# Performance work log

Measured on AMD Instinct MI355X. Metric: run time of the kernel, lower is better.

Reference implementation:

```python
import jax, jax.numpy as jnp
import numpy as np

# static config
B, L, D = 2, 4096, 1024
H, G, WIN = 16, 2, 256
HD = D // H            # 64
KV = G * HD            # 128 (k/v proj width)
E, HID, TOPK = 8, 1024, 2
ENT_W, MAX_USE, EPS = 0.05, 0.4, 1e-8


def setup_inputs() -> dict:
    key = jax.random.key(0)
    ks = jax.random.split(key, 16)
    s = 0.02
    return {
        "x": jax.random.normal(ks[0], (B, L, D), jnp.float32),
        "Wq": jax.random.normal(ks[1], (D, D), jnp.float32) * s,
        "bq": jnp.zeros((D,), jnp.float32),
        "Wk": jax.random.normal(ks[2], (D, KV), jnp.float32) * s,
        "bk": jnp.zeros((KV,), jnp.float32),
        "Wv": jax.random.normal(ks[3], (D, KV), jnp.float32) * s,
        "bv": jnp.zeros((KV,), jnp.float32),
        "Wo": jax.random.normal(ks[4], (D, D), jnp.float32) * s,
        "bo": jnp.zeros((D,), jnp.float32),
        "ln1_g": jnp.ones((D,), jnp.float32),
        "ln1_b": jnp.zeros((D,), jnp.float32),
        "ln2_g": jnp.ones((D,), jnp.float32),
        "ln2_b": jnp.zeros((D,), jnp.float32),
        "Wg": jax.random.normal(ks[5], (D, E), jnp.float32) * 0.01,
        "bg": jnp.zeros((E,), jnp.float32),
        "We": jax.random.normal(ks[6], (E, D, HID), jnp.float32) * s,
        "be": jnp.zeros((E, HID), jnp.float32),
    }


def _layernorm(x, g, b):
    mu = jnp.mean(x, axis=-1, keepdims=True)
    var = jnp.var(x, axis=-1, keepdims=True)
    return (x - mu) * jax.lax.rsqrt(var + 1e-5) * g + b


def _local_attn(x, Wq, bq, Wk, bk, Wv, bv, Wo, bo):
    # overlapping sliding-window bidirectional GQA attention (dropout off / eval)
    Bx, Lx, _ = x.shape
    pad = (-Lx) % WIN
    xp = jnp.pad(x, ((0, 0), (0, pad), (0, 0)))
    Lp = Lx + pad
    q = (xp @ Wq + bq).reshape(Bx, Lp, H, HD).transpose(0, 2, 1, 3)   # [B,H,Lp,hd]
    k = (xp @ Wk + bk).reshape(Bx, Lp, G, HD).transpose(0, 2, 1, 3)   # [B,G,Lp,hd]
    v = (xp @ Wv + bv).reshape(Bx, Lp, G, HD).transpose(0, 2, 1, 3)
    stride = WIN // 2
    nw = (Lp - WIN) // stride + 1
    win_idx = (np.arange(nw)[:, None] * stride + np.arange(WIN)[None, :])
    qw = q[:, :, win_idx]
    kw = k[:, :, win_idx]
    vw = v[:, :, win_idx]
    rep = H // G
    # torch .repeat tiles kv groups: head h uses group h % G, i.e. h = r*G + g
    qw = qw.reshape(Bx, rep, G, nw, WIN, HD)
    scores = jnp.einsum('brgnqd,bgnkd->brgnqk', qw, kw) / np.sqrt(HD)
    attn = jax.nn.softmax(scores, axis=-1)
    o = jnp.einsum('brgnqk,bgnkd->brgnqd', attn, vw)
    o = o.reshape(Bx, H, nw, WIN, HD).transpose(0, 2, 3, 1, 4).reshape(Bx, nw * WIN, D)
    o = o[:, :Lx]                             # truncate concatenated windows to L
    return o @ Wo + bo


def _moe(x, Wg, bg, We, be):
    Bx, Lx, _ = x.shape
    xf = x.reshape(-1, D)                     # [N,D]
    N = xf.shape[0]
    probs = jax.nn.softmax(xf @ Wg + bg, axis=-1)          # [N,E]
    entropy = -jnp.sum(probs * jnp.log(probs + EPS), axis=-1).mean()
    ent_loss = ENT_W * entropy
    topk_p, topk_i = jax.lax.top_k(probs, TOPK)            # [N,K]
    # dense grouped-GEMM reference for top-k dispatch/combine
    all_out = jnp.einsum('nd,edh->neh', xf, We) + be       # [N,E,HID]
    wts = jnp.zeros((N, E), xf.dtype).at[jnp.arange(N)[:, None], topk_i].add(topk_p)
    out = jnp.einsum('ne,neh->nh', wts, all_out)           # [N,HID]
    counts = jnp.zeros((E,), xf.dtype).at[topk_i.reshape(-1)].add(1.0)
    usage = counts / (N + EPS)
    penalty = jnp.sum(jax.nn.relu(usage - MAX_USE))
    return out.reshape(Bx, Lx, HID), ent_loss + penalty


def reference(x, Wq, bq, Wk, bk, Wv, bv, Wo, bo, ln1_g, ln1_b, ln2_g, ln2_b, Wg, bg, We, be):
    h = x + _local_attn(_layernorm(x, ln1_g, ln1_b), Wq, bq, Wk, bk, Wv, bv, Wo, bo)
    moe_out, aux = _moe(_layernorm(h, ln2_g, ln2_b), Wg, bg, We, be)
    out = h + moe_out
    return out, aux
```

## Files before the change

### kernel.cpp

```cpp
#include <hip/hip_runtime.h>
#include <hip/hip_bf16.h>
#include <stdint.h>

typedef __attribute__((ext_vector_type(8))) short bf16x8;
typedef __attribute__((ext_vector_type(8))) _Float16 f16x8;
typedef __attribute__((ext_vector_type(4))) _Float16 f16x4;
typedef __attribute__((ext_vector_type(4))) float f32x4;

__device__ __forceinline__ short f2bf(float f) {
  __hip_bfloat16 h = __float2bfloat16(f);
  union { __hip_bfloat16 h; short s; } u; u.h = h; return u.s;
}

__device__ __forceinline__ unsigned pk2(float a, float b) {
  union { _Float16 h; unsigned short s; } ua, ub;
  ua.h = (_Float16)a; ub.h = (_Float16)b;
  return (unsigned)ua.s | ((unsigned)ub.s << 16);
}

__device__ __forceinline__ void gld16(const void* g, void* l) {
  __builtin_amdgcn_global_load_lds((const __attribute__((address_space(1))) void*)g,
                                   (__attribute__((address_space(3))) void*)l, 16, 0, 0);
}

__device__ __forceinline__ float wave_sum64(float v) {
  #pragma unroll
  for (int off = 1; off < 64; off <<= 1) v += __shfl_xor(v, off);
  return v;
}
__device__ __forceinline__ double wave_sum64d(double v) {
  #pragma unroll
  for (int off = 1; off < 64; off <<= 1) v += __shfl_xor(v, off);
  return v;
}

__global__ __launch_bounds__(256) void ln_split(const float* __restrict__ x,
    const float* __restrict__ g, const float* __restrict__ b,
    _Float16* __restrict__ xh, _Float16* __restrict__ xl) {
  int t = blockIdx.x, tid = threadIdx.x;
  const float4 v = ((const float4*)(x + (size_t)t * 1024))[tid];
  float s = v.x + v.y + v.z + v.w;
  float s2 = v.x*v.x + v.y*v.y + v.z*v.z + v.w*v.w;
  s = wave_sum64(s); s2 = wave_sum64(s2);
  __shared__ float pa[4], pb[4];
  int wid = tid >> 6, lane = tid & 63;
  if (lane == 0) { pa[wid] = s; pb[wid] = s2; }
  __syncthreads();
  float S = pa[0]+pa[1]+pa[2]+pa[3], S2 = pb[0]+pb[1]+pb[2]+pb[3];
  float mu = S * (1.f/1024.f);
  float var = S2 * (1.f/1024.f) - mu*mu;
  float rs = rsqrtf(var + 1e-5f);
  const float4 gv = ((const float4*)g)[tid];
  const float4 bv = ((const float4*)b)[tid];
  float4 o;
  o.x = (v.x-mu)*rs*gv.x + bv.x; o.y = (v.y-mu)*rs*gv.y + bv.y;
  o.z = (v.z-mu)*rs*gv.z + bv.z; o.w = (v.w-mu)*rs*gv.w + bv.w;
  f16x4 hv, lv;
  hv.x = (_Float16)o.x; lv.x = (_Float16)((o.x - (float)hv.x)*2048.f);
  hv.y = (_Float16)o.y; lv.y = (_Float16)((o.y - (float)hv.y)*2048.f);
  hv.z = (_Float16)o.z; lv.z = (_Float16)((o.z - (float)hv.z)*2048.f);
  hv.w = (_Float16)o.w; lv.w = (_Float16)((o.w - (float)hv.w)*2048.f);
  *(f16x4*)&xh[(size_t)t*1024 + tid*4] = hv;
  *(f16x4*)&xl[(size_t)t*1024 + tid*4] = lv;
}

__global__ __launch_bounds__(256) void ln_bf16(const float* __restrict__ x,
    const float* __restrict__ g, const float* __restrict__ b, short* __restrict__ out,
    float2* __restrict__ murs) {
  int t = blockIdx.x, tid = threadIdx.x;
  const float4 v = ((const float4*)(x + (size_t)t * 1024))[tid];
  float s = v.x + v.y + v.z + v.w;
  float s2 = v.x*v.x + v.y*v.y + v.z*v.z + v.w*v.w;
  s = wave_sum64(s); s2 = wave_sum64(s2);
  __shared__ float pa[4], pb[4];
  int wid = tid >> 6, lane = tid & 63;
  if (lane == 0) { pa[wid] = s; pb[wid] = s2; }
  __syncthreads();
  float S = pa[0]+pa[1]+pa[2]+pa[3], S2 = pb[0]+pb[1]+pb[2]+pb[3];
  float mu = S * (1.f/1024.f);
  float var = S2 * (1.f/1024.f) - mu*mu;
  float rs = rsqrtf(var + 1e-5f);
  if (tid == 0) murs[t] = make_float2(mu, rs);
  const float4 gv = ((const float4*)g)[tid];
  const float4 bv = ((const float4*)b)[tid];
  short4 o;
  o.x = f2bf((v.x-mu)*rs*gv.x + bv.x); o.y = f2bf((v.y-mu)*rs*gv.y + bv.y);
  o.z = f2bf((v.z-mu)*rs*gv.z + bv.z); o.w = f2bf((v.w-mu)*rs*gv.w + bv.w);
  ((short4*)(out + (size_t)t * 1024))[tid] = o;
}

__global__ void t_w_f16(const float* __restrict__ src, int srcN,
                        _Float16* __restrict__ dh, _Float16* __restrict__ dl, int dstRow0) {
  __shared__ float tile[32][33];
  int kt = blockIdx.x, nt = blockIdx.y;
  int tx = threadIdx.x, ty = threadIdx.y;
  #pragma unroll
  for (int i = 0; i < 4; i++)
    tile[ty + 8*i][tx] = src[(size_t)(kt*32 + ty + 8*i)*srcN + nt*32 + tx];
  __syncthreads();
  #pragma unroll
  for (int i = 0; i < 4; i++) {
    float v = tile[tx][ty + 8*i];
    _Float16 h = (_Float16)v;
    _Float16 l = (_Float16)((v - (float)h) * 2048.0f);
    size_t o = (size_t)(dstRow0 + nt*32 + ty + 8*i)*1024 + kt*32 + tx;
    dh[o] = h; dl[o] = l;
  }
}

template<int MODE>
__global__ __launch_bounds__(256, 3) void gemm_dma(
    const _Float16* __restrict__ Agh, const _Float16* __restrict__ Agl,
    const _Float16* __restrict__ BTh, const _Float16* __restrict__ BTl,
    const float* __restrict__ b0, const float* __restrict__ b1, const float* __restrict__ b2,
    const float* __restrict__ resid,
    float* __restrict__ out0, float* __restrict__ out1, float* __restrict__ out2) {
  int m0 = blockIdx.x * 64;
  int y = blockIdx.y;
  int n0 = y * 128;
  float* dst; const float* biasp; int dcol0, ld;
  if (MODE == 0) {
    if (y < 8)      { dst = out0; biasp = b0 + y*128; dcol0 = y*128; ld = 1024; }
    else if (y == 8){ dst = out1; biasp = b1; dcol0 = 0; ld = 128; }
    else            { dst = out2; biasp = b2; dcol0 = 0; ld = 128; }
  } else            { dst = out0; biasp = b0 + y*128; dcol0 = y*128; ld = 1024; }

  __shared__ _Float16 AhS[2][2048];
  __shared__ _Float16 AlS[2][2048];
  __shared__ _Float16 BhS[2][4096];
  __shared__ _Float16 BlS[2][4096];
  int tid = threadIdx.x;
  int lane = tid & 63, w = tid >> 6;
  int wm = (w & 1) * 32, wn = (w >> 1) * 64;
  int l15 = lane & 15, quad = lane >> 4;

  int Pa = tid;
  int cA = (Pa & 3) ^ ((Pa >> 4) & 3);
  size_t gA = (size_t)(m0 + (Pa >> 2)) * 1024 + cA * 8;
  int Pb0 = tid, Pb1 = tid + 256;
  int cB0 = (Pb0 & 3) ^ ((Pb0 >> 4) & 3);
  int cB1 = (Pb1 & 3) ^ ((Pb1 >> 4) & 3);
  size_t gB0 = (size_t)(n0 + (Pb0 >> 2)) * 1024 + cB0 * 8;
  size_t gB1 = (size_t)(n0 + (Pb1 >> 2)) * 1024 + cB1 * 8;

  f32x4 accM[2][4] = {};
  f32x4 accC[2][4] = {};

  gld16(Agh + gA, &AhS[0][Pa*8]);
  gld16(Agl + gA, &AlS[0][Pa*8]);
  gld16(BTh + gB0, &BhS[0][Pb0*8]);
  gld16(BTh + gB1, &BhS[0][Pb1*8]);
  gld16(BTl + gB0, &BlS[0][Pb0*8]);
  gld16(BTl + gB1, &BlS[0][Pb1*8]);
  __syncthreads();

  int cur = 0;
  for (int it = 0; it < 32; ++it) {
    if (it < 31) {
      int kb = (it + 1) * 32;
      int nb = cur ^ 1;
      gld16(Agh + gA + kb, &AhS[nb][Pa*8]);
      gld16(Agl + gA + kb, &AlS[nb][Pa*8]);
      gld16(BTh + gB0 + kb, &BhS[nb][Pb0*8]);
      gld16(BTh + gB1 + kb, &BhS[nb][Pb1*8]);
      gld16(BTl + gB0 + kb, &BlS[nb][Pb0*8]);
      gld16(BTl + gB1 + kb, &BlS[nb][Pb1*8]);
    }
    f16x8 bh[4], bl[4];
    #pragma unroll
    for (int nt = 0; nt < 4; nt++) {
      int row = wn + nt*16 + l15;
      int pc = quad ^ ((row >> 2) & 3);
      bh[nt] = *(const f16x8*)&BhS[cur][row*32 + pc*8];
      bl[nt] = *(const f16x8*)&BlS[cur][row*32 + pc*8];
    }
    #pragma unroll
    for (int mt = 0; mt < 2; mt++) {
      int row = wm + mt*16 + l15;
      int pc = quad ^ ((row >> 2) & 3);
      f16x8 ah = *(const f16x8*)&AhS[cur][row*32 + pc*8];
      f16x8 al = *(const f16x8*)&AlS[cur][row*32 + pc*8];
      #pragma unroll
      for (int nt = 0; nt < 4; nt++) {
        accM[mt][nt] = __builtin_amdgcn_mfma_f32_16x16x32_f16(ah, bh[nt], accM[mt][nt], 0, 0, 0);
        accC[mt][nt] = __builtin_amdgcn_mfma_f32_16x16x32_f16(ah, bl[nt], accC[mt][nt], 0, 0, 0);
        accC[mt][nt] = __builtin_amdgcn_mfma_f32_16x16x32_f16(al, bh[nt], accC[mt][nt], 0, 0, 0);
      }
    }
    __syncthreads();
    cur ^= 1;
  }

  const float inv2048 = 1.0f / 2048.0f;
  #pragma unroll
  for (int mt = 0; mt < 2; mt++)
    #pragma unroll
    for (int r = 0; r < 4; r++) {
      int row = m0 + wm + mt*16 + quad*4 + r;
      #pragma unroll
      for (int nt = 0; nt < 4; nt++) {
        int c = wn + nt*16 + l15;
        float v = accM[mt][nt][r] + accC[mt][nt][r]*inv2048 + biasp[c];
        if (MODE == 1) v += resid[(size_t)row*1024 + dcol0 + c];
        dst[(size_t)row*ld + dcol0 + c] = v;
      }
    }
}

__global__ __launch_bounds__(256, 2) void attn_mfma(
    const float* __restrict__ Qs, const float* __restrict__ Kf, const float* __restrict__ Vf,
    _Float16* __restrict__ Oh, _Float16* __restrict__ Ol) {
  int qb = blockIdx.x, n = blockIdx.y;
  int b = blockIdx.z >> 4, h = blockIdx.z & 15;
  int g = h & 1;
  int tid = threadIdx.x;
  int lane = tid & 63, w = tid >> 6;
  int l15 = lane & 15, quad = lane >> 4;

  __shared__ __align__(16) char smem[70912];
  _Float16* Vt = (_Float16*)smem;
  _Float16* Qh = (_Float16*)(smem + 33792);
  _Float16* Ql = (_Float16*)(smem + 43008);
  _Float16* Kh = (_Float16*)(smem + 52224);
  _Float16* Kl = (_Float16*)(smem + 61440);
  _Float16* Pm = (_Float16*)(smem + 33792);
  float*   linv = (float*)(smem + 70656);

  int qtok0 = b*4096 + n*128 + qb*64;
  int key0  = b*4096 + n*128;

  #pragma unroll
  for (int i = 0; i < 4; i++) {
    int idx = tid + 256*i;
    int row = idx >> 4, c4 = idx & 15;
    float4 v = *(const float4*)&Qs[(size_t)(qtok0+row)*1024 + h*64 + c4*4];
    f16x4 hv, lv;
    hv.x = (_Float16)v.x; lv.x = (_Float16)(v.x - (float)hv.x);
    hv.y = (_Float16)v.y; lv.y = (_Float16)(v.y - (float)hv.y);
    hv.z = (_Float16)v.z; lv.z = (_Float16)(v.z - (float)hv.z);
    hv.w = (_Float16)v.w; lv.w = (_Float16)(v.w - (float)hv.w);
    *(f16x4*)&Qh[row*72 + c4*4] = hv;
    *(f16x4*)&Ql[row*72 + c4*4] = lv;
  }
  {
    int kk = tid >> 4, dd = tid & 15;
    #pragma unroll
    for (int i = 0; i < 8; i++) {
      int p = i*16 + kk;
      float4 v0 = *(const float4*)&Vf[(size_t)(key0 + 2*p    )*128 + g*64 + dd*4];
      float4 v1 = *(const float4*)&Vf[(size_t)(key0 + 2*p + 1)*128 + g*64 + dd*4];
      *(unsigned*)&Vt[(dd*4+0)*264 + 2*p] = pk2(v0.x, v1.x);
      *(unsigned*)&Vt[(dd*4+1)*264 + 2*p] = pk2(v0.y, v1.y);
      *(unsigned*)&Vt[(dd*4+2)*264 + 2*p] = pk2(v0.z, v1.z);
      *(unsigned*)&Vt[(dd*4+3)*264 + 2*p] = pk2(v0.w, v1.w);
    }
  }
  __syncthreads();

  f16x8 qh[2], ql[2];
  {
    int qrow = (w*16 + l15)*72;
    qh[0] = *(const f16x8*)&Qh[qrow + quad*8];
    qh[1] = *(const f16x8*)&Qh[qrow + 32 + quad*8];
    ql[0] = *(const f16x8*)&Ql[qrow + quad*8];
    ql[1] = *(const f16x8*)&Ql[qrow + 32 + quad*8];
  }

  f32x4 S[16];
  #pragma unroll
  for (int t = 0; t < 16; t++) S[t] = (f32x4){0.f,0.f,0.f,0.f};

  for (int c = 0; c < 4; c++) {
    if (c) __syncthreads();
    #pragma unroll
    for (int i = 0; i < 4; i++) {
      int idx = tid + 256*i;
      int row = idx >> 4, c4 = idx & 15;
      float4 v = *(const float4*)&Kf[(size_t)(key0 + c*64 + row)*128 + g*64 + c4*4];
      f16x4 hv, lv;
      hv.x = (_Float16)v.x; lv.x = (_Float16)(v.x - (float)hv.x);
      hv.y = (_Float16)v.y; lv.y = (_Float16)(v.y - (float)hv.y);
      hv.z = (_Float16)v.z; lv.z = (_Float16)(v.z - (float)hv.z);
      hv.w = (_Float16)v.w; lv.w = (_Float16)(v.w - (float)hv.w);
      *(f16x4*)&Kh[row*72 + c4*4] = hv;
      *(f16x4*)&Kl[row*72 + c4*4] = lv;
    }
    __syncthreads();
    #pragma unroll
    for (int t = 0; t < 4; t++) {
      int krow = (t*16 + l15)*72;
      f16x8 kh0 = *(const f16x8*)&Kh[krow + quad*8];
      f16x8 kh1 = *(const f16x8*)&Kh[krow + 32 + quad*8];
      f16x8 kl0 = *(const f16x8*)&Kl[krow + quad*8];
      f16x8 kl1 = *(const f16x8*)&Kl[krow + 32 + quad*8];
      int ti = c*4 + t;
      S[ti] = __builtin_amdgcn_mfma_f32_16x16x32_f16(qh[0], kh0, S[ti], 0, 0, 0);
      S[ti] = __builtin_amdgcn_mfma_f32_16x16x32_f16(ql[0], kh0, S[ti], 0, 0, 0);
      S[ti] = __builtin_amdgcn_mfma_f32_16x16x32_f16(qh[0], kl0, S[ti], 0, 0, 0);
      S[ti] = __builtin_amdgcn_mfma_f32_16x16x32_f16(qh[1], kh1, S[ti], 0, 0, 0);
      S[ti] = __builtin_amdgcn_mfma_f32_16x16x32_f16(ql[1], kh1, S[ti], 0, 0, 0);
      S[ti] = __builtin_amdgcn_mfma_f32_16x16x32_f16(qh[1], kl1, S[ti], 0, 0, 0);
    }
  }

  float lrow[4];
  #pragma unroll
  for (int r = 0; r < 4; r++) {
    float mx = S[0][r];
    #pragma unroll
    for (int t = 1; t < 16; t++) mx = fmaxf(mx, S[t][r]);
    mx = fmaxf(mx, __shfl_xor(mx, 1)); mx = fmaxf(mx, __shfl_xor(mx, 2));
    mx = fmaxf(mx, __shfl_xor(mx, 4)); mx = fmaxf(mx, __shfl_xor(mx, 8));
    float sum = 0.f;
    #pragma unroll
    for (int t = 0; t < 16; t++) {
      float e = __expf((S[t][r] - mx) * 0.125f);
      S[t][r] = e; sum += e;
    }
    sum += __shfl_xor(sum, 1); sum += __shfl_xor(sum, 2);
    sum += __shfl_xor(sum, 4); sum += __shfl_xor(sum, 8);
    lrow[r] = sum;
  }
  if (l15 == 0) {
    #pragma unroll
    for (int r = 0; r < 4; r++) linv[w*16 + quad*4 + r] = 1.f / lrow[r];
  }
  __syncthreads();

  #pragma unroll
  for (int r = 0; r < 4; r++) {
    int q = w*16 + quad*4 + r;
    bool mine = (l15 & 1) ? (r >= 2) : (r < 2);
    #pragma unroll
    for (int t = 0; t < 16; t++) {
      float own = S[t][r];
      float oth = __shfl_xor(own, 1);
      if (mine) {
        float e0 = (l15 & 1) ? oth : own;
        float e1 = (l15 & 1) ? own : oth;
        *(unsigned*)&Pm[q*264 + t*16 + (l15 & ~1)] = pk2(e0, e1);
      }
    }
  }
  __syncthreads();

  f32x4 O[4];
  #pragma unroll
  for (int t = 0; t < 4; t++) O[t] = (f32x4){0.f,0.f,0.f,0.f};
  {
    int prow = (w*16 + l15)*264;
    #pragma unroll
    for (int ks = 0; ks < 8; ks++) {
      f16x8 pa = *(const f16x8*)&Pm[prow + ks*32 + quad*8];
      #pragma unroll
      for (int t = 0; t < 4; t++) {
        f16x8 vb = *(const f16x8*)&Vt[(t*16 + l15)*264 + ks*32 + quad*8];
        O[t] = __builtin_amdgcn_mfma_f32_16x16x32_f16(pa, vb, O[t], 0, 0, 0);
      }
    }
  }

  #pragma unroll
  for (int r = 0; r < 4; r++) {
    int qlocal = w*16 + quad*4 + r;
    float inv = linv[qlocal];
    int orow = b*4096 + n*256 + qb*64 + qlocal;
    #pragma unroll
    for (int t = 0; t < 4; t++) {
      float o = O[t][r] * inv;
      _Float16 oh = (_Float16)o;
      _Float16 ol = (_Float16)((o - (float)oh) * 2048.f);
      size_t oo = (size_t)orow*1024 + h*64 + t*16 + l15;
      Oh[oo] = oh; Ol[oo] = ol;
    }
  }
}

__global__ __launch_bounds__(256) void gating_logits(
    const float* __restrict__ h, const float2* __restrict__ murs,
    const float* __restrict__ g2, const float* __restrict__ b2,
    const float* __restrict__ Wg, const float* __restrict__ bg,
    int* __restrict__ e1e2, float2* __restrict__ p12, float* __restrict__ entArr) {
  int tid = threadIdx.x, lane = tid & 63, wid = tid >> 6;
  int tok = blockIdx.x*4 + wid;
  const float* row = h + (size_t)tok * 1024;
  float2 mr = murs[tok];
  double mu = (double)mr.x, rs = (double)mr.y;
  double acc[8] = {};
  #pragma unroll
  for (int q = 0; q < 4; q++) {
    float4 xv = ((const float4*)row)[lane*4 + q];
    float4 gv = ((const float4*)g2)[lane*4 + q];
    float4 bv = ((const float4*)b2)[lane*4 + q];
    float xs[4] = {xv.x, xv.y, xv.z, xv.w};
    float gs[4] = {gv.x, gv.y, gv.z, gv.w};
    float bs[4] = {bv.x, bv.y, bv.z, bv.w};
    #pragma unroll
    for (int j = 0; j < 4; j++) {
      int i = lane*16 + q*4 + j;
      double xn = ((double)xs[j] - mu) * rs * (double)gs[j] + (double)bs[j];
      const float4 w0 = *(const float4*)&Wg[(size_t)i*8];
      const float4 w1 = *(const float4*)&Wg[(size_t)i*8 + 4];
      acc[0] += xn*(double)w0.x; acc[1] += xn*(double)w0.y;
      acc[2] += xn*(double)w0.z; acc[3] += xn*(double)w0.w;
      acc[4] += xn*(double)w1.x; acc[5] += xn*(double)w1.y;
      acc[6] += xn*(double)w1.z; acc[7] += xn*(double)w1.w;
    }
  }
  #pragma unroll
  for (int e = 0; e < 8; e++) acc[e] = wave_sum64d(acc[e]) + (double)bg[e];
  int e1 = 0;
  #pragma unroll
  for (int e = 1; e < 8; e++) if (acc[e] > acc[e1]) e1 = e;
  int e2 = (e1 == 0) ? 1 : 0;
  #pragma unroll
  for (int e = 0; e < 8; e++) if (e != e1 && acc[e] > acc[e2]) e2 = e;
  float lf[8];
  #pragma unroll
  for (int e = 0; e < 8; e++) lf[e] = (float)acc[e];
  float mx = lf[0];
  #pragma unroll
  for (int e = 1; e < 8; e++) mx = fmaxf(mx, lf[e]);
  float ex[8], Z = 0.f;
  #pragma unroll
  for (int e = 0; e < 8; e++) { ex[e] = __expf(lf[e] - mx); Z += ex[e]; }
  float invZ = 1.f / Z, ent = 0.f;
  float p[8];
  #pragma unroll
  for (int e = 0; e < 8; e++) { p[e] = ex[e]*invZ; ent -= p[e]*__logf(p[e] + 1e-8f); }
  if (lane == 0) {
    e1e2[tok] = e1 | (e2 << 8);
    p12[tok]  = make_float2(p[e1], p[e2]);
    entArr[tok] = ent;
  }
}

__global__ __launch_bounds__(128) void scatter_kernel(
    const int* __restrict__ e1e2, const float2* __restrict__ p12,
    int* __restrict__ cnt, int* __restrict__ bucket, float* __restrict__ bucketP,
    int* __restrict__ bucketS) {
  __shared__ int lcnt[8], base[8];
  int tid = threadIdx.x;
  if (tid < 8) lcnt[tid] = 0;
  __syncthreads();
  int tok = blockIdx.x*128 + tid;
  int ee = e1e2[tok];
  int e1 = ee & 255, e2 = ee >> 8;
  float2 p = p12[tok];
  int o1 = atomicAdd(&lcnt[e1], 1);
  int o2 = atomicAdd(&lcnt[e2], 1);
  __syncthreads();
  if (tid < 8) base[tid] = atomicAdd(&cnt[tid], lcnt[tid]);
  __syncthreads();
  int i1 = base[e1] + o1;
  bucket[e1*8192 + i1] = tok; bucketP[e1*8192 + i1] = p.x; bucketS[e1*8192 + i1] = 0;
  int i2 = base[e2] + o2;
  bucket[e2*8192 + i2] = tok; bucketP[e2*8192 + i2] = p.y; bucketS[e2*8192 + i2] = 1;
}

__global__ __launch_bounds__(256) void aux_kernel(const float* __restrict__ entArr,
    const int* __restrict__ cnt, float* __restrict__ auxOut) {
  int tid = threadIdx.x;
  float s = 0.f;
  for (int i = tid; i < 8192; i += 256) s += entArr[i];
  s = wave_sum64(s);
  __shared__ float pa[4];
  if ((tid & 63) == 0) pa[tid >> 6] = s;
  __syncthreads();
  if (tid == 0) {
    float tot = pa[0]+pa[1]+pa[2]+pa[3];
    float entMean = tot / 8192.f;
    float pen = 0.f;
    for (int e = 0; e < 8; e++) {
      float usage = (float)cnt[e] / (8192.f + 1e-8f);
      pen += fmaxf(usage - 0.4f, 0.f);
    }
    auxOut[0] = 0.05f * entMean + pen;
  }
}

__global__ void transpose_We(const float* __restrict__ We, short* __restrict__ WeT) {
  int e = blockIdx.z;
  __shared__ float tile[32][33];
  int kt = blockIdx.x, nt = blockIdx.y;
  int tx = threadIdx.x, ty = threadIdx.y;
  const float* src = We + (size_t)e * 1048576;
  short* dst = WeT + (size_t)e * 1048576;
  #pragma unroll
  for (int i = 0; i < 4; i++)
    tile[ty + 8*i][tx] = src[(size_t)(kt*32 + ty + 8*i)*1024 + nt*32 + tx];
  __syncthreads();
  #pragma unroll
  for (int i = 0; i < 4; i++)
    dst[(size_t)(nt*32 + ty + 8*i)*1024 + kt*32 + tx] = f2bf(tile[tx][ty + 8*i]);
}

__global__ __launch_bounds__(256) void moe_gemm(
    const short* __restrict__ hln, const short* __restrict__ WeT,
    const float* __restrict__ be, const int* __restrict__ cnt,
    const int* __restrict__ bucket, const float* __restrict__ bucketP,
    const int* __restrict__ bucketS,
    float* __restrict__ slot0, float* __restrict__ slot1) {
  int e = blockIdx.z;
  int count = cnt[e];
  int mtile = blockIdx.x;
  if (mtile * 128 >= count) return;
  int n0 = blockIdx.y * 128;
  __shared__ short As[8192];
  __shared__ short Bs[8192];
  __shared__ int   toks[128];
  __shared__ float pws[128];
  __shared__ int   sls[128];
  int tid = threadIdx.x;
  if (tid < 128) {
    int idx = mtile*128 + tid;
    int ic = idx < count ? idx : count - 1;
    toks[tid] = bucket[e*8192 + ic];
    pws[tid]  = bucketP[e*8192 + ic];
    sls[tid]  = bucketS[e*8192 + ic];
  }
  __syncthreads();
  int lane = tid & 63, w = tid >> 6;
  int wm = (w & 1) * 64, wn = (w >> 1) * 64;
  int l15 = lane & 15, quad = lane >> 4;
  const short* Bt = WeT + (size_t)e * 1048576;

  size_t goA[4], goB[4];
  int Pc[4];
  #pragma unroll
  for (int i = 0; i < 4; i++) {
    int P = (i*4 + w)*64 + lane;
    int row = P >> 3;
    int c = (P & 7) ^ (row & 7);
    Pc[i] = P;
    goA[i] = (size_t)toks[row]*1024 + c*8;
    goB[i] = (size_t)(n0 + row)*1024 + c*8;
  }

  f32x4 acc[4][4] = {};
  for (int kb = 0; kb < 1024; kb += 64) {
    __syncthreads();
    #pragma unroll
    for (int i = 0; i < 4; i++) {
      gld16(hln + goA[i] + kb, &As[Pc[i]*8]);
      gld16(Bt  + goB[i] + kb, &Bs[Pc[i]*8]);
    }
    __syncthreads();
    #pragma unroll
    for (int ks = 0; ks < 2; ks++) {
      bf16x8 af[4], bfr[4];
      #pragma unroll
      for (int nt = 0; nt < 4; nt++) {
        int row = wn + nt*16 + l15;
        int pc = (ks*4 + quad) ^ (row & 7);
        bfr[nt] = *(const bf16x8*)&Bs[row*64 + pc*8];
      }
      #pragma unroll
      for (int mt = 0; mt < 4; mt++) {
        int row = wm + mt*16 + l15;
        int pc = (ks*4 + quad) ^ (row & 7);
        af[mt] = *(const bf16x8*)&As[row*64 + pc*8];
        #pragma unroll
        for (int nt = 0; nt < 4; nt++)
          acc[mt][nt] = __builtin_amdgcn_mfma_f32_16x16x32_bf16(af[mt], bfr[nt], acc[mt][nt], 0, 0, 0);
      }
    }
  }
  #pragma unroll
  for (int mt = 0; mt < 4; mt++) {
    #pragma unroll
    for (int r = 0; r < 4; r++) {
      int m = wm + mt*16 + quad*4 + r;
      if (mtile*128 + m < count) {
        int tok = toks[m];
        float pp = pws[m];
        float* dst = sls[m] ? slot1 : slot0;
        #pragma unroll
        for (int nt = 0; nt < 4; nt++) {
          int col = n0 + wn + nt*16 + l15;
          dst[(size_t)tok*1024 + col] = pp * (acc[mt][nt][r] + be[e*1024 + col]);
        }
      }
    }
  }
}

__global__ __launch_bounds__(256) void final_add(float* __restrict__ out,
    const float* __restrict__ s0, const float* __restrict__ s1) {
  const int total = 8388608 / 4;
  for (int i = blockIdx.x*256 + threadIdx.x; i < total; i += gridDim.x*256) {
    float4 a = ((float4*)out)[i];
    const float4 x0 = ((const float4*)s0)[i];
    const float4 x1 = ((const float4*)s1)[i];
    a.x += x0.x + x1.x; a.y += x0.y + x1.y; a.z += x0.z + x1.z; a.w += x0.w + x1.w;
    ((float4*)out)[i] = a;
  }
}

extern "C" void kernel_launch(void* const* d_in, const int* in_sizes, int n_in,
                              void* d_out, int out_size, void* d_ws, size_t ws_size,
                              hipStream_t stream) {
  const float* x    = (const float*)d_in[0];
  const float* Wq   = (const float*)d_in[1];
  const float* bq   = (const float*)d_in[2];
  const float* Wk   = (const float*)d_in[3];
  const float* bk   = (const float*)d_in[4];
  const float* Wv   = (const float*)d_in[5];
  const float* bv   = (const float*)d_in[6];
  const float* Wo   = (const float*)d_in[7];
  const float* bo   = (const float*)d_in[8];
  const float* ln1g = (const float*)d_in[9];
  const float* ln1b = (const float*)d_in[10];
  const float* ln2g = (const float*)d_in[11];
  const float* ln2b = (const float*)d_in[12];
  const float* Wg   = (const float*)d_in[13];
  const float* bg   = (const float*)d_in[14];
  const float* We   = (const float*)d_in[15];
  const float* be   = (const float*)d_in[16];
  float* out = (float*)d_out;

  char* ws = (char*)d_ws;
  size_t off = 0;
  auto alloc = [&](size_t bytes) { char* p = ws + off; off += (bytes + 255) & ~(size_t)255; return p; };
  _Float16* xh  = (_Float16*)alloc(16777216);
  _Float16* xl  = (_Float16*)alloc(16777216);
  float* Qs    = (float*)alloc(33554432);
  float* Kf    = (float*)alloc(4194304);
  float* Vf    = (float*)alloc(4194304);
  short* WeT   = (short*)alloc(16777216);
  float* slot0 = (float*)alloc(33554432);
  float* slot1 = (float*)alloc(33554432);
  int*   bucket  = (int*)alloc(262144);
  float* bucketP = (float*)alloc(262144);
  int*   bucketS = (int*)alloc(262144);
  int*   cnt     = (int*)alloc(256);
  float* entArr  = (float*)alloc(32768);
  int*   e1e2    = (int*)alloc(32768);
  float2* p12    = (float2*)alloc(65536);
  float2* murs   = (float2*)alloc(65536);
  _Float16* Oh = xh;
  _Float16* Ol = xl;
  short* hln   = (short*)Qs;
  _Float16* WoTh    = (_Float16*)slot0;
  _Float16* WoTl    = (_Float16*)(slot0 + 524288);
  _Float16* BTqkv_h = (_Float16*)slot1;
  _Float16* BTqkv_l = (_Float16*)((char*)slot1 + 2621440);

  hipMemsetAsync(cnt, 0, 256, stream);
  t_w_f16<<<dim3(32, 32), dim3(32, 8), 0, stream>>>(Wq, 1024, BTqkv_h, BTqkv_l, 0);
  t_w_f16<<<dim3(32, 4),  dim3(32, 8), 0, stream>>>(Wk, 128,  BTqkv_h, BTqkv_l, 1024);
  t_w_f16<<<dim3(32, 4),  dim3(32, 8), 0, stream>>>(Wv, 128,  BTqkv_h, BTqkv_l, 1152);
  t_w_f16<<<dim3(32, 32), dim3(32, 8), 0, stream>>>(Wo, 1024, WoTh, WoTl, 0);
  transpose_We<<<dim3(32,32,8), dim3(32,8), 0, stream>>>(We, WeT);

  ln_split<<<8192, 256, 0, stream>>>(x, ln1g, ln1b, xh, xl);
  gemm_dma<0><<<dim3(128,10), 256, 0, stream>>>(xh, xl, BTqkv_h, BTqkv_l, bq, bk, bv,
                                                nullptr, Qs, Kf, Vf);
  attn_mfma<<<dim3(4,16,32), 256, 0, stream>>>(Qs, Kf, Vf, Oh, Ol);
  gemm_dma<1><<<dim3(128,8), 256, 0, stream>>>(Oh, Ol, WoTh, WoTl, bo, nullptr, nullptr,
                                               x, out, nullptr, nullptr);
  ln_bf16<<<8192, 256, 0, stream>>>(out, ln2g, ln2b, hln, murs);
  gating_logits<<<2048, 256, 0, stream>>>(out, murs, ln2g, ln2b, Wg, bg, e1e2, p12, entArr);
  scatter_kernel<<<64, 128, 0, stream>>>(e1e2, p12, cnt, bucket, bucketP, bucketS);
  aux_kernel<<<1, 256, 0, stream>>>(entArr, cnt, out + 8388608);
  moe_gemm<<<dim3(64,8,8), 256, 0, stream>>>(hln, WeT, be, cnt, bucket, bucketP, bucketS, slot0, slot1);
  final_add<<<2048, 256, 0, stream>>>(out, slot0, slot1);
}
```

Baseline: 564.0 us.

## Double-buffer MoE GEMM LDS tiles with K=32 steps and prefetch

```diff
diff --git a/kernel.cpp b/kernel.cpp
--- a/kernel.cpp
+++ b/kernel.cpp
@@ -495,7 +495,7 @@
     dst[(size_t)(nt*32 + ty + 8*i)*1024 + kt*32 + tx] = f2bf(tile[tx][ty + 8*i]);
 }
 
-__global__ __launch_bounds__(256) void moe_gemm(
+__global__ __launch_bounds__(256, 4) void moe_gemm(
     const short* __restrict__ hln, const short* __restrict__ WeT,
     const float* __restrict__ be, const int* __restrict__ cnt,
     const int* __restrict__ bucket, const float* __restrict__ bucketP,
@@ -506,8 +506,8 @@
   int mtile = blockIdx.x;
   if (mtile * 128 >= count) return;
   int n0 = blockIdx.y * 128;
-  __shared__ short As[8192];
-  __shared__ short Bs[8192];
+  __shared__ short As[2][4096];
+  __shared__ short Bs[2][4096];
   __shared__ int   toks[128];
   __shared__ float pws[128];
   __shared__ int   sls[128];
@@ -525,47 +525,52 @@
   int l15 = lane & 15, quad = lane >> 4;
   const short* Bt = WeT + (size_t)e * 1048576;
 
-  size_t goA[4], goB[4];
-  int Pc[4];
-  #pragma unroll
-  for (int i = 0; i < 4; i++) {
-    int P = (i*4 + w)*64 + lane;
-    int row = P >> 3;
-    int c = (P & 7) ^ (row & 7);
-    Pc[i] = P;
-    goA[i] = (size_t)toks[row]*1024 + c*8;
-    goB[i] = (size_t)(n0 + row)*1024 + c*8;
-  }
+  int P0 = tid, P1 = tid + 256;
+  int c0 = (P0 & 3) ^ ((P0 >> 4) & 3);
+  int c1 = (P1 & 3) ^ ((P1 >> 4) & 3);
+  size_t gA0 = (size_t)toks[P0 >> 2] * 1024 + c0 * 8;
+  size_t gA1 = (size_t)toks[P1 >> 2] * 1024 + c1 * 8;
+  size_t gB0 = (size_t)(n0 + (P0 >> 2)) * 1024 + c0 * 8;
+  size_t gB1 = (size_t)(n0 + (P1 >> 2)) * 1024 + c1 * 8;
 
   f32x4 acc[4][4] = {};
-  for (int kb = 0; kb < 1024; kb += 64) {
+
+  gld16(hln + gA0, &As[0][P0*8]);
+  gld16(hln + gA1, &As[0][P1*8]);
+  gld16(Bt  + gB0, &Bs[0][P0*8]);
+  gld16(Bt  + gB1, &Bs[0][P1*8]);
+  __syncthreads();
+
+  int cur = 0;
+  for (int it = 0; it < 32; ++it) {
+    if (it < 31) {
+      int kb = (it + 1) * 32;
+      int nb = cur ^ 1;
+      gld16(hln + gA0 + kb, &As[nb][P0*8]);
+      gld16(hln + gA1 + kb, &As[nb][P1*8]);
+      gld16(Bt  + gB0 + kb, &Bs[nb][P0*8]);
+      gld16(Bt  + gB1 + kb, &Bs[nb][P1*8]);
+    }
+    bf16x8 af[4], bfr[4];
+    #pragma unroll
+    for (int nt = 0; nt < 4; nt++) {
+      int row = wn + nt*16 + l15;
+      int pc = quad ^ ((row >> 2) & 3);
+      bfr[nt] = *(const bf16x8*)&Bs[cur][row*32 + pc*8];
+    }
+    #pragma unroll
+    for (int mt = 0; mt < 4; mt++) {
+      int row = wm + mt*16 + l15;
+      int pc = quad ^ ((row >> 2) & 3);
+      af[mt] = *(const bf16x8*)&As[cur][row*32 + pc*8];
+      #pragma unroll
+      for (int nt = 0; nt < 4; nt++)
+        acc[mt][nt] = __builtin_amdgcn_mfma_f32_16x16x32_bf16(af[mt], bfr[nt], acc[mt][nt], 0, 0, 0);
+    }
     __syncthreads();
-    #pragma unroll
-    for (int i = 0; i < 4; i++) {
-      gld16(hln + goA[i] + kb, &As[Pc[i]*8]);
-      gld16(Bt  + goB[i] + kb, &Bs[Pc[i]*8]);
-    }
-    __syncthreads();
-    #pragma unroll
-    for (int ks = 0; ks < 2; ks++) {
-      bf16x8 af[4], bfr[4];
-      #pragma unroll
-      for (int nt = 0; nt < 4; nt++) {
-        int row = wn + nt*16 + l15;
-        int pc = (ks*4 + quad) ^ (row & 7);
-        bfr[nt] = *(const bf16x8*)&Bs[row*64 + pc*8];
-      }
-      #pragma unroll
-      for (int mt = 0; mt < 4; mt++) {
-        int row = wm + mt*16 + l15;
-        int pc = (ks*4 + quad) ^ (row & 7);
-        af[mt] = *(const bf16x8*)&As[row*64 + pc*8];
-        #pragma unroll
-        for (int nt = 0; nt < 4; nt++)
-          acc[mt][nt] = __builtin_amdgcn_mfma_f32_16x16x32_bf16(af[mt], bfr[nt], acc[mt][nt], 0, 0, 0);
-      }
-    }
-  }
+    cur ^= 1;
+  }
+
   #pragma unroll
   for (int mt = 0; mt < 4; mt++) {
     #pragma unroll
```

Measured after the change: 570.5 us. No clear change (+1.1%).
